# Optimization experiments

Measured on AMD Instinct MI355X. Metric: run time of the kernel, lower is better.

The kernel has to match this reference:

```python
import jax, jax.numpy as jnp
import numpy as np

LAGS = 2
LATENT = 64          # latent_size; number of tiny per-dim MLPs
HID = 64             # hidden_dim of each MLP2
SLOPE = 0.2          # LeakyReLU negative slope
IN_DIM = LAGS * LATENT + 1  # 129: flattened lags + current value of dim i


def setup_inputs() -> dict:
    key = jax.random.key(0)
    k0, k1, k2, k3, k4 = jax.random.split(key, 5)
    B, LEN = 32, 512
    x = jax.random.normal(k0, (B, LEN + LAGS, LATENT), jnp.float32)
    # Stacked per-latent MLP2 params (num_layers=1):
    #   Linear(IN_DIM -> HID) + LeakyReLU(0.2) + Linear(HID -> 1)
    s1 = float(1.0 / np.sqrt(IN_DIM))
    s2 = float(1.0 / np.sqrt(HID))
    W1 = jax.random.uniform(k1, (LATENT, HID, IN_DIM), jnp.float32, -s1, s1)
    b1 = jax.random.uniform(k2, (LATENT, HID), jnp.float32, -s1, s1)
    W2 = jax.random.uniform(k3, (LATENT, HID), jnp.float32, -s2, s2)
    b2 = jax.random.uniform(k4, (LATENT,), jnp.float32, -s2, s2)
    return {"x": x, "W1": W1, "b1": b1, "W2": W2, "b2": b2}


def reference(x, W1, b1, W2, b2):
    B, T, xd = x.shape
    length = T - LAGS
    N = B * length
    # torch unfold(dim=1, size=LAGS+1, step=1).transpose(2,3) -> [B, length, LAGS+1, xd]
    idx = jnp.arange(length)[:, None] + jnp.arange(LAGS + 1)[None, :]
    win = x[:, idx]                                   # [B, length, LAGS+1, xd]
    lagsx = win[:, :, :-1].reshape(N, LAGS * xd)      # [N, LAGS*xd]
    xt = win[:, :, -1].reshape(N, xd)                 # [N, xd] current values per latent dim
    # gs[i] input = concat(lagsx, xt[:, i:i+1]); batch all latent dims at once.
    W1_lags = W1[:, :, :-1]                           # [L, H, LAGS*xd]
    w1_t = W1[:, :, -1]                               # [L, H] weight on the appended x_t column
    pre = (jnp.einsum('nd,lhd->nlh', lagsx, W1_lags)
           + xt[:, :, None] * w1_t[None]
           + b1[None])                                # [N, L, H]
    act = jnp.where(pre >= 0, pre, SLOPE * pre)       # LeakyReLU(0.2)
    residuals = jnp.einsum('nlh,lh->nl', act, W2) + b2[None]   # [N, L]
    # Analytic last column of the per-sample Jacobian (d residual_i / d x_t_i):
    dact = jnp.where(pre >= 0, 1.0, SLOPE)
    J_last = jnp.einsum('lh,nlh,lh->nl', W2, dact, w1_t)       # [N, L]
    logabsdet = jnp.sum(jnp.log(jnp.abs(J_last)), axis=-1)     # [N]
    return residuals.reshape(B, length, xd), logabsdet.reshape(B, length)
```

## Files before the change

kernel.cpp:

```cpp
#include <hip/hip_runtime.h>
#include <math.h>

#define SLOPE  0.2f
#define NB     32
#define LEN    512
#define LATENT 64
#define HID    64
#define IN_DIM 129
#define TROWS  514
#define NTOT   (NB * LEN)

typedef __attribute__((ext_vector_type(8)))  short bf16x8;
typedef __attribute__((ext_vector_type(16))) float f32x16;
typedef __attribute__((ext_vector_type(4)))  float f32x4;

struct alignas(8) US4 { unsigned short x, y, z, w; };

__device__ inline void bsplit(float v, unsigned short& hi, unsigned short& lo) {
    unsigned int u  = __builtin_bit_cast(unsigned int, v);
    unsigned int hb = (u + 0x7fffu + ((u >> 16) & 1u)) >> 16;
    hi = (unsigned short)hb;
    float fh = __builtin_bit_cast(float, hb << 16);
    float r  = v - fh;
    unsigned int u2 = __builtin_bit_cast(unsigned int, r);
    lo = (unsigned short)((u2 + 0x7fffu + ((u2 >> 16) & 1u)) >> 16);
}

__global__ __launch_bounds__(256)
void conv_w1(const float* __restrict__ W1g, unsigned short* __restrict__ W1f,
             float* __restrict__ W1t, float* __restrict__ out_lad) {
    const int idx = blockIdx.x * 256 + threadIdx.x;
    if (idx < NTOT) out_lad[idx] = 0.f;
    const int row  = idx >> 4;
    const int o    = idx & 15;
    const int ks   = o >> 1, hi32 = o & 1;
    const int l    = row >> 6, h = row & 63;
    const int i    = h >> 5,  r32 = h & 31;
    const int lane = hi32 * 32 + r32;
    const float* src = W1g + (size_t)row * IN_DIM + o * 8;
    unsigned short hh[8], ll[8];
    #pragma unroll
    for (int e = 0; e < 8; ++e) bsplit(src[e], hh[e], ll[e]);
    const size_t base = (size_t)l * 16384 + (size_t)i * 8192 + (size_t)ks * 1024
                      + (size_t)lane * 8;
    *reinterpret_cast<US4*>(W1f + base)       = US4{hh[0], hh[1], hh[2], hh[3]};
    *reinterpret_cast<US4*>(W1f + base + 4)   = US4{hh[4], hh[5], hh[6], hh[7]};
    *reinterpret_cast<US4*>(W1f + base + 512) = US4{ll[0], ll[1], ll[2], ll[3]};
    *reinterpret_cast<US4*>(W1f + base + 516) = US4{ll[4], ll[5], ll[6], ll[7]};
    if (o == 15) W1t[row] = src[8];
}

__global__ __launch_bounds__(256, 4)
void fused_mfma(const float* __restrict__ xg,
                const float* __restrict__ b1g, const float* __restrict__ W2g,
                const float* __restrict__ b2g,
                const unsigned short* __restrict__ W1f,
                const float* __restrict__ W1t,
                float* __restrict__ out_res, float* __restrict__ out_lad)
{
    __shared__ unsigned short sXh[34][72];
    __shared__ unsigned short sXl[34][72];
    __shared__ float sJ[32][4];

    const int tid   = threadIdx.x;
    const int tile  = blockIdx.x & 511;
    const int lhalf = blockIdx.x >> 9;
    const int pt    = tile >> 4;
    const int s     = tile & 15;
    const size_t xrow0 = (size_t)pt * TROWS + s * 32;
    const size_t nbase = (size_t)tile * 32;

    for (int i = tid; i < 34 * 16; i += 256) {
        const int row = i >> 4, c4 = (i & 15) << 2;
        const float4 v = *reinterpret_cast<const float4*>(
            xg + (xrow0 + row) * LATENT + c4);
        unsigned short h0,h1,h2,h3, l0,l1,l2,l3;
        bsplit(v.x, h0, l0); bsplit(v.y, h1, l1);
        bsplit(v.z, h2, l2); bsplit(v.w, h3, l3);
        *reinterpret_cast<US4*>(&sXh[row][c4]) = US4{h0, h1, h2, h3};
        *reinterpret_cast<US4*>(&sXl[row][c4]) = US4{l0, l1, l2, l3};
    }
    __syncthreads();

    const int wn   = tid >> 6;
    const int lane = tid & 63;
    const int r32  = lane & 31;
    const int hi32 = lane >> 5;

    float jlog = 0.f, jprod = 1.f;

    #pragma unroll 1
    for (int q = 0; q < 8; ++q) {
        const int l = lhalf * 32 + q * 4 + wn;
        const unsigned short* A0 = W1f + (size_t)l * 16384 + (size_t)lane * 8;

        f32x16 acc[2];
        #pragma unroll
        for (int i = 0; i < 2; ++i)
            #pragma unroll
            for (int r = 0; r < 16; ++r) acc[i][r] = 0.f;

        #pragma unroll
        for (int ks = 0; ks < 8; ++ks) {
            const int lag = ks >> 2;
            const int cc  = (ks & 3) * 16 + hi32 * 8;
            const unsigned short* p0 = A0 + ks * 1024;
            bf16x8 awh[2], awl[2];
            #pragma unroll
            for (int i = 0; i < 2; ++i) {
                awh[i] = *reinterpret_cast<const bf16x8*>(p0 + i * 8192);
                awl[i] = *reinterpret_cast<const bf16x8*>(p0 + i * 8192 + 512);
            }
            const bf16x8 bxh = *reinterpret_cast<const bf16x8*>(&sXh[r32 + lag][cc]);
            const bf16x8 bxl = *reinterpret_cast<const bf16x8*>(&sXl[r32 + lag][cc]);
            #pragma unroll
            for (int i = 0; i < 2; ++i) {
                acc[i] = __builtin_amdgcn_mfma_f32_32x32x16_bf16(awh[i], bxh, acc[i], 0, 0, 0);
                acc[i] = __builtin_amdgcn_mfma_f32_32x32x16_bf16(awh[i], bxl, acc[i], 0, 0, 0);
                acc[i] = __builtin_amdgcn_mfma_f32_32x32x16_bf16(awl[i], bxh, acc[i], 0, 0, 0);
            }
        }

        const float xt0 = xg[(xrow0 + 2 + r32) * LATENT + l];
        float res0 = 0.f, jp0 = 0.f, jc = 0.f;
        #pragma unroll
        for (int i = 0; i < 2; ++i)
            #pragma unroll
            for (int g = 0; g < 4; ++g) {
                const int h0 = l * HID + i * 32 + hi32 * 4 + g * 8;
                const f32x4 wt = *reinterpret_cast<const f32x4*>(W1t + h0);
                const f32x4 w2 = *reinterpret_cast<const f32x4*>(W2g + h0);
                const f32x4 b1 = *reinterpret_cast<const f32x4*>(b1g + h0);
                #pragma unroll
                for (int m = 0; m < 4; ++m) {
                    const float c0 = w2[m] * wt[m];
                    jc += c0;
                    const float pre0 = fmaf(xt0, wt[m], acc[i][g * 4 + m] + b1[m]);
                    res0 += w2[m] * fmaxf(pre0, SLOPE * pre0);
                    jp0 += (pre0 >= 0.f) ? c0 : 0.f;
                }
            }

        res0 += __shfl_xor(res0, 32);
        jp0  += __shfl_xor(jp0, 32);
        jc   += __shfl_xor(jc, 32);
        const float jac = SLOPE * jc + (1.f - SLOPE) * jp0;

        if (hi32 == 0)
            out_res[(nbase + r32) * LATENT + l] = res0 + b2g[l];

        jprod *= jac;
        if ((q & 3) == 3) {
            jlog += logf(fabsf(jprod));
            jprod = 1.f;
        }
    }

    if (hi32 == 0) sJ[r32][wn] = jlog;
    __syncthreads();
    if (tid < 32) {
        const float part = sJ[tid][0] + sJ[tid][1] + sJ[tid][2] + sJ[tid][3];
        atomicAdd(&out_lad[nbase + tid], part);
    }
}

extern "C" void kernel_launch(void* const* d_in, const int* in_sizes, int n_in,
                              void* d_out, int out_size, void* d_ws, size_t ws_size,
                              hipStream_t stream) {
    const float* xg  = (const float*)d_in[0];
    const float* W1g = (const float*)d_in[1];
    const float* b1g = (const float*)d_in[2];
    const float* W2g = (const float*)d_in[3];
    const float* b2g = (const float*)d_in[4];

    float* out_res = (float*)d_out;
    float* out_lad = out_res + (size_t)NTOT * LATENT;

    float*          W1t = (float*)d_ws;
    unsigned short* W1f = (unsigned short*)(W1t + 4096);

    conv_w1<<<256, 256, 0, stream>>>(W1g, W1f, W1t, out_lad);

    dim3 grid(1024);
    fused_mfma<<<grid, 256, 0, stream>>>(xg, b1g, W2g, b2g, W1f, W1t,
                                         out_res, out_lad);
}
```

Before: 143.5 us.

## Fold x_t and bias into extra MFMA, precompute Jacobian constants, split latents four ways

```diff
diff --git a/kernel.cpp b/kernel.cpp
--- a/kernel.cpp
+++ b/kernel.cpp
@@ -14,7 +14,8 @@
 typedef __attribute__((ext_vector_type(16))) float f32x16;
 typedef __attribute__((ext_vector_type(4)))  float f32x4;
 
-struct alignas(8) US4 { unsigned short x, y, z, w; };
+struct alignas(8)  US4 { unsigned short x, y, z, w; };
+struct alignas(16) US8 { unsigned short s[8]; };
 
 __device__ inline void bsplit(float v, unsigned short& hi, unsigned short& lo) {
     unsigned int u  = __builtin_bit_cast(unsigned int, v);
@@ -27,46 +28,68 @@
 }
 
 __global__ __launch_bounds__(256)
-void conv_w1(const float* __restrict__ W1g, unsigned short* __restrict__ W1f,
-             float* __restrict__ W1t, float* __restrict__ out_lad) {
-    const int idx = blockIdx.x * 256 + threadIdx.x;
-    if (idx < NTOT) out_lad[idx] = 0.f;
-    const int row  = idx >> 4;
-    const int o    = idx & 15;
-    const int ks   = o >> 1, hi32 = o & 1;
-    const int l    = row >> 6, h = row & 63;
-    const int i    = h >> 5,  r32 = h & 31;
-    const int lane = hi32 * 32 + r32;
-    const float* src = W1g + (size_t)row * IN_DIM + o * 8;
-    unsigned short hh[8], ll[8];
+void conv_w1(const float* __restrict__ W1g, const float* __restrict__ b1g,
+             const float* __restrict__ W2g,
+             unsigned short* __restrict__ W1f, unsigned int* __restrict__ Aext,
+             float* __restrict__ C0, float* __restrict__ Jc,
+             float* __restrict__ out_lad) {
+    const int t = blockIdx.x * 256 + threadIdx.x;
+    if (t < NTOT) out_lad[t] = 0.f;
+    if (t < 4096) C0[t] = W2g[t] * W1g[(size_t)t * IN_DIM + 128];
+    if (t < 64) {
+        float s = 0.f;
+        for (int h = 0; h < 64; ++h) {
+            const int row = t * 64 + h;
+            s += W2g[row] * W1g[(size_t)row * IN_DIM + 128];
+        }
+        Jc[t] = s;
+    }
+    if (t < 8192) {
+        const int r32p = t & 31, partp = (t >> 5) & 1;
+        const int ip = (t >> 6) & 1, lp = t >> 7;
+        const int row = lp * 64 + ip * 32 + r32p;
+        unsigned short wh, wl, bh, bl;
+        bsplit(W1g[(size_t)row * IN_DIM + 128], wh, wl);
+        bsplit(b1g[row], bh, bl);
+        Aext[t] = partp ? ((unsigned int)wl | ((unsigned int)bl << 16))
+                        : ((unsigned int)wh | ((unsigned int)bh << 16));
+    }
+    const int lane = t & 63;
+    const int part = (t >> 6) & 1;
+    const int ks   = (t >> 7) & 7;
+    const int i    = (t >> 10) & 1;
+    const int l    = t >> 11;
+    const int hi32 = lane >> 5, r32 = lane & 31;
+    const int row  = l * 64 + i * 32 + r32;
+    const int k0   = ks * 16 + hi32 * 8;
+    const float* src = W1g + (size_t)row * IN_DIM + k0;
+    US8 v;
     #pragma unroll
-    for (int e = 0; e < 8; ++e) bsplit(src[e], hh[e], ll[e]);
-    const size_t base = (size_t)l * 16384 + (size_t)i * 8192 + (size_t)ks * 1024
-                      + (size_t)lane * 8;
-    *reinterpret_cast<US4*>(W1f + base)       = US4{hh[0], hh[1], hh[2], hh[3]};
-    *reinterpret_cast<US4*>(W1f + base + 4)   = US4{hh[4], hh[5], hh[6], hh[7]};
-    *reinterpret_cast<US4*>(W1f + base + 512) = US4{ll[0], ll[1], ll[2], ll[3]};
-    *reinterpret_cast<US4*>(W1f + base + 516) = US4{ll[4], ll[5], ll[6], ll[7]};
-    if (o == 15) W1t[row] = src[8];
+    for (int e = 0; e < 8; ++e) {
+        unsigned short h, lo;
+        bsplit(src[e], h, lo);
+        v.s[e] = part ? lo : h;
+    }
+    *reinterpret_cast<US8*>(W1f + (size_t)t * 8) = v;
 }
 
 __global__ __launch_bounds__(256, 4)
 void fused_mfma(const float* __restrict__ xg,
-                const float* __restrict__ b1g, const float* __restrict__ W2g,
-                const float* __restrict__ b2g,
+                const float* __restrict__ W2g, const float* __restrict__ b2g,
                 const unsigned short* __restrict__ W1f,
-                const float* __restrict__ W1t,
+                const unsigned int* __restrict__ Aext,
+                const float* __restrict__ C0, const float* __restrict__ Jc,
                 float* __restrict__ out_res, float* __restrict__ out_lad)
 {
     __shared__ unsigned short sXh[34][72];
     __shared__ unsigned short sXl[34][72];
     __shared__ float sJ[32][4];
 
-    const int tid   = threadIdx.x;
-    const int tile  = blockIdx.x & 511;
-    const int lhalf = blockIdx.x >> 9;
-    const int pt    = tile >> 4;
-    const int s     = tile & 15;
+    const int tid  = threadIdx.x;
+    const int tile = blockIdx.x & 511;
+    const int lq   = blockIdx.x >> 9;
+    const int pt   = tile >> 4;
+    const int s    = tile & 15;
     const size_t xrow0 = (size_t)pt * TROWS + s * 32;
     const size_t nbase = (size_t)tile * 32;
 
@@ -90,8 +113,8 @@
     float jlog = 0.f, jprod = 1.f;
 
     #pragma unroll 1
-    for (int q = 0; q < 8; ++q) {
-        const int l = lhalf * 32 + q * 4 + wn;
+    for (int q = 0; q < 4; ++q) {
+        const int l = lq * 16 + q * 4 + wn;
         const unsigned short* A0 = W1f + (size_t)l * 16384 + (size_t)lane * 8;
 
         f32x16 acc[2];
@@ -121,41 +144,59 @@
             }
         }
 
-        const float xt0 = xg[(xrow0 + 2 + r32) * LATENT + l];
-        float res0 = 0.f, jp0 = 0.f, jc = 0.f;
+        {
+            const int abase = l * 128 + r32;
+            const unsigned int avh0 = Aext[abase];
+            const unsigned int avl0 = Aext[abase + 32];
+            const unsigned int avh1 = Aext[abase + 64];
+            const unsigned int avl1 = Aext[abase + 96];
+            const unsigned short xh = sXh[2 + r32][l];
+            const unsigned short xl = sXl[2 + r32][l];
+            bf16x8 aeh0 = {0,0,0,0,0,0,0,0}, ael0 = {0,0,0,0,0,0,0,0};
+            bf16x8 aeh1 = {0,0,0,0,0,0,0,0}, ael1 = {0,0,0,0,0,0,0,0};
+            bf16x8 beh  = {0,0,0,0,0,0,0,0}, bel  = {0,0,0,0,0,0,0,0};
+            if (hi32 == 0) {
+                aeh0[0] = (short)(avh0 & 0xffff); aeh0[1] = (short)(avh0 >> 16);
+                ael0[0] = (short)(avl0 & 0xffff); ael0[1] = (short)(avl0 >> 16);
+                aeh1[0] = (short)(avh1 & 0xffff); aeh1[1] = (short)(avh1 >> 16);
+                ael1[0] = (short)(avl1 & 0xffff); ael1[1] = (short)(avl1 >> 16);
+                beh[0] = (short)xh; beh[1] = (short)0x3F80;
+                bel[0] = (short)xl;
+            }
+            acc[0] = __builtin_amdgcn_mfma_f32_32x32x16_bf16(aeh0, beh, acc[0], 0, 0, 0);
+            acc[0] = __builtin_amdgcn_mfma_f32_32x32x16_bf16(aeh0, bel, acc[0], 0, 0, 0);
+            acc[0] = __builtin_amdgcn_mfma_f32_32x32x16_bf16(ael0, beh, acc[0], 0, 0, 0);
+            acc[1] = __builtin_amdgcn_mfma_f32_32x32x16_bf16(aeh1, beh, acc[1], 0, 0, 0);
+            acc[1] = __builtin_amdgcn_mfma_f32_32x32x16_bf16(aeh1, bel, acc[1], 0, 0, 0);
+            acc[1] = __builtin_amdgcn_mfma_f32_32x32x16_bf16(ael1, beh, acc[1], 0, 0, 0);
+        }
+
+        float res0 = 0.f, jp0 = 0.f;
         #pragma unroll
         for (int i = 0; i < 2; ++i)
             #pragma unroll
             for (int g = 0; g < 4; ++g) {
                 const int h0 = l * HID + i * 32 + hi32 * 4 + g * 8;
-                const f32x4 wt = *reinterpret_cast<const f32x4*>(W1t + h0);
                 const f32x4 w2 = *reinterpret_cast<const f32x4*>(W2g + h0);
-                const f32x4 b1 = *reinterpret_cast<const f32x4*>(b1g + h0);
+                const f32x4 c0 = *reinterpret_cast<const f32x4*>(C0 + h0);
                 #pragma unroll
                 for (int m = 0; m < 4; ++m) {
-                    const float c0 = w2[m] * wt[m];
-                    jc += c0;
-                    const float pre0 = fmaf(xt0, wt[m], acc[i][g * 4 + m] + b1[m]);
-                    res0 += w2[m] * fmaxf(pre0, SLOPE * pre0);
-                    jp0 += (pre0 >= 0.f) ? c0 : 0.f;
+                    const float pre = acc[i][g * 4 + m];
+                    res0 += w2[m] * fmaxf(pre, SLOPE * pre);
+                    jp0  += (pre >= 0.f) ? c0[m] : 0.f;
                 }
             }
 
         res0 += __shfl_xor(res0, 32);
         jp0  += __shfl_xor(jp0, 32);
-        jc   += __shfl_xor(jc, 32);
-        const float jac = SLOPE * jc + (1.f - SLOPE) * jp0;
+        const float jac = SLOPE * Jc[l] + (1.f - SLOPE) * jp0;
 
         if (hi32 == 0)
             out_res[(nbase + r32) * LATENT + l] = res0 + b2g[l];
-
         jprod *= jac;
-        if ((q & 3) == 3) {
-            jlog += logf(fabsf(jprod));
-            jprod = 1.f;
-        }
-    }
-
+    }
+
+    jlog = logf(fabsf(jprod));
     if (hi32 == 0) sJ[r32][wn] = jlog;
     __syncthreads();
     if (tid < 32) {
@@ -176,12 +217,14 @@
     float* out_res = (float*)d_out;
     float* out_lad = out_res + (size_t)NTOT * LATENT;
 
-    float*          W1t = (float*)d_ws;
-    unsigned short* W1f = (unsigned short*)(W1t + 4096);
-
-    conv_w1<<<256, 256, 0, stream>>>(W1g, W1f, W1t, out_lad);
-
-    dim3 grid(1024);
-    fused_mfma<<<grid, 256, 0, stream>>>(xg, b1g, W2g, b2g, W1f, W1t,
+    float*          C0   = (float*)d_ws;
+    float*          Jc   = C0 + 4096;
+    unsigned int*   Aext = (unsigned int*)(Jc + 64);
+    unsigned short* W1f  = (unsigned short*)(Aext + 8192);
+
+    conv_w1<<<512, 256, 0, stream>>>(W1g, b1g, W2g, W1f, Aext, C0, Jc, out_lad);
+
+    dim3 grid(2048);
+    fused_mfma<<<grid, 256, 0, stream>>>(xg, W2g, b2g, W1f, Aext, C0, Jc,
                                          out_res, out_lad);
 }
```

After: 169.9 us. 1.18x slower.

## Merge weight conversion and main kernel into one cooperative launch with grid sync

Applied to the files above, without the earlier changes.

```diff
diff --git a/kernel.cpp b/kernel.cpp
--- a/kernel.cpp
+++ b/kernel.cpp
@@ -1,5 +1,8 @@
 #include <hip/hip_runtime.h>
+#include <hip/hip_cooperative_groups.h>
 #include <math.h>
+
+namespace cg = cooperative_groups;
 
 #define SLOPE  0.2f
 #define NB     32
@@ -14,7 +17,8 @@
 typedef __attribute__((ext_vector_type(16))) float f32x16;
 typedef __attribute__((ext_vector_type(4)))  float f32x4;
 
-struct alignas(8) US4 { unsigned short x, y, z, w; };
+struct alignas(8)  US4 { unsigned short x, y, z, w; };
+struct alignas(16) US8 { unsigned short s[8]; };
 
 __device__ inline void bsplit(float v, unsigned short& hi, unsigned short& lo) {
     unsigned int u  = __builtin_bit_cast(unsigned int, v);
@@ -26,43 +30,49 @@
     lo = (unsigned short)((u2 + 0x7fffu + ((u2 >> 16) & 1u)) >> 16);
 }
 
-__global__ __launch_bounds__(256)
-void conv_w1(const float* __restrict__ W1g, unsigned short* __restrict__ W1f,
-             float* __restrict__ W1t, float* __restrict__ out_lad) {
-    const int idx = blockIdx.x * 256 + threadIdx.x;
-    if (idx < NTOT) out_lad[idx] = 0.f;
-    const int row  = idx >> 4;
-    const int o    = idx & 15;
-    const int ks   = o >> 1, hi32 = o & 1;
-    const int l    = row >> 6, h = row & 63;
-    const int i    = h >> 5,  r32 = h & 31;
-    const int lane = hi32 * 32 + r32;
-    const float* src = W1g + (size_t)row * IN_DIM + o * 8;
-    unsigned short hh[8], ll[8];
-    #pragma unroll
-    for (int e = 0; e < 8; ++e) bsplit(src[e], hh[e], ll[e]);
-    const size_t base = (size_t)l * 16384 + (size_t)i * 8192 + (size_t)ks * 1024
-                      + (size_t)lane * 8;
-    *reinterpret_cast<US4*>(W1f + base)       = US4{hh[0], hh[1], hh[2], hh[3]};
-    *reinterpret_cast<US4*>(W1f + base + 4)   = US4{hh[4], hh[5], hh[6], hh[7]};
-    *reinterpret_cast<US4*>(W1f + base + 512) = US4{ll[0], ll[1], ll[2], ll[3]};
-    *reinterpret_cast<US4*>(W1f + base + 516) = US4{ll[4], ll[5], ll[6], ll[7]};
-    if (o == 15) W1t[row] = src[8];
-}
-
 __global__ __launch_bounds__(256, 4)
-void fused_mfma(const float* __restrict__ xg,
-                const float* __restrict__ b1g, const float* __restrict__ W2g,
-                const float* __restrict__ b2g,
-                const unsigned short* __restrict__ W1f,
-                const float* __restrict__ W1t,
-                float* __restrict__ out_res, float* __restrict__ out_lad)
+void fused_all(const float* xg, const float* W1g, const float* b1g,
+               const float* W2g, const float* b2g,
+               unsigned short* W1f, float* W1t,
+               float* out_res, float* out_lad, int phase)
 {
     __shared__ unsigned short sXh[34][72];
     __shared__ unsigned short sXl[34][72];
     __shared__ float sJ[32][4];
 
-    const int tid   = threadIdx.x;
+    const int tid = threadIdx.x;
+
+    if (phase != 1) {
+        const int t = blockIdx.x * 256 + tid;
+        if (t < NTOT) out_lad[t] = 0.f;
+        if (t < 4096) W1t[t] = W1g[(size_t)t * IN_DIM + 128];
+        if (t < 131072) {
+            const int lane = t & 63;
+            const int part = (t >> 6) & 1;
+            const int ks   = (t >> 7) & 7;
+            const int i    = (t >> 10) & 1;
+            const int l    = t >> 11;
+            const int hi32 = lane >> 5, r32 = lane & 31;
+            const int row  = l * 64 + i * 32 + r32;
+            const int k0   = ks * 16 + hi32 * 8;
+            const float* src = W1g + (size_t)row * IN_DIM + k0;
+            US8 v;
+            #pragma unroll
+            for (int e = 0; e < 8; ++e) {
+                unsigned short h, lo;
+                bsplit(src[e], h, lo);
+                v.s[e] = part ? lo : h;
+            }
+            *reinterpret_cast<US8*>(W1f + (size_t)t * 8) = v;
+        }
+    }
+
+    if (phase == 2) {
+        __threadfence();
+        cg::this_grid().sync();
+    }
+    if (phase == 0) return;
+
     const int tile  = blockIdx.x & 511;
     const int lhalf = blockIdx.x >> 9;
     const int pt    = tile >> 4;
@@ -179,9 +189,18 @@
     float*          W1t = (float*)d_ws;
     unsigned short* W1f = (unsigned short*)(W1t + 4096);
 
-    conv_w1<<<256, 256, 0, stream>>>(W1g, W1f, W1t, out_lad);
-
-    dim3 grid(1024);
-    fused_mfma<<<grid, 256, 0, stream>>>(xg, b1g, W2g, b2g, W1f, W1t,
-                                         out_res, out_lad);
+    int phase2 = 2;
+    void* args[] = { (void*)&xg, (void*)&W1g, (void*)&b1g, (void*)&W2g,
+                     (void*)&b2g, (void*)&W1f, (void*)&W1t,
+                     (void*)&out_res, (void*)&out_lad, (void*)&phase2 };
+
+    hipError_t err = hipLaunchCooperativeKernel((const void*)fused_all,
+                                                dim3(1024), dim3(256),
+                                                args, 0, stream);
+    if (err != hipSuccess) {
+        fused_all<<<1024, 256, 0, stream>>>(xg, W1g, b1g, W2g, b2g,
+                                            W1f, W1t, out_res, out_lad, 0);
+        fused_all<<<1024, 256, 0, stream>>>(xg, W1g, b1g, W2g, b2g,
+                                            W1f, W1t, out_res, out_lad, 1);
+    }
 }
```

Result: slower. 348.8 us (+143.1%).
